# Kernel optimization log

Measured on AMD Instinct MI355X. Metric: run time of the kernel, lower is better.

## Reference

```python
import jax, jax.numpy as jnp
import numpy as np

TEMPERATURE = 1.0


def setup_inputs() -> dict:
    key = jax.random.key(0)
    kq, kk, kv = jax.random.split(key, 3)
    shape = (2, 16, 2048, 64)  # B, H, L, D
    q = jax.random.normal(kq, shape, dtype=jnp.float32)
    k = jax.random.normal(kk, shape, dtype=jnp.float32)
    v = jax.random.normal(kv, shape, dtype=jnp.float32)
    return {"q": q, "k": k, "v": v}


def reference(q, k, v):
    # q, k, v: [B, H, L, D]
    L = q.shape[2]
    # scores: [B, H, L, L]; note: divided by temperature, NOT sqrt(D), per source
    scores = jnp.einsum("bhqd,bhkd->bhqk", q, k) / TEMPERATURE
    # causal mask: position j > i masked with -inf
    causal = jnp.tril(jnp.ones((L, L), dtype=bool))  # True = keep
    scores = jnp.where(causal, scores, -jnp.inf)
    attn = jax.nn.softmax(scores, axis=-1)
    out = jnp.einsum("bhqk,bhkd->bhqd", attn, v)
    return out
```

## Files before the change

kernel.cpp:

```cpp
#include <hip/hip_runtime.h>
#include <math.h>


typedef __attribute__((ext_vector_type(8))) _Float16 f16x8;
typedef __attribute__((ext_vector_type(4))) _Float16 f16x4;
typedef __attribute__((ext_vector_type(4))) float f32x4;

constexpr int Lq = 2048;
constexpr int Dd = 64;
constexpr int KT = 64;
constexpr int THREADS = 256;
constexpr int CHUNK = 64;
constexpr int NCHUNK = Lq / CHUNK;
constexpr int PAIRS = NCHUNK / 2;

#define SWZB(row, bcol) ((((row) * 128) + (bcol)) ^ (((row) & 7) << 4))

__global__ __launch_bounds__(THREADS)
void causal_attn_mfma(const float* __restrict__ Q, const float* __restrict__ K,
                      const float* __restrict__ V, float* __restrict__ O) {
  __shared__ char ks[2][KT * 128];
  __shared__ char vt[2][Dd * 128];
  __shared__ char pl[4][16 * 128];

  const int tid  = threadIdx.x;
  const int lane = tid & 63;
  const int wv   = tid >> 6;
  const int l15  = lane & 15;
  const int g    = lane >> 4;
  const int kg = tid & 15;
  const int dq = tid >> 4;

  const int bh = blockIdx.x / PAIRS;
  const int pr = blockIdx.x % PAIRS;
  const size_t base = (size_t)bh * Lq * Dd;
  const float* Qb = Q + base;
  const float* Kb = K + base;
  const float* Vb = V + base;
  float*       Ob = O + base;
  char* pw = pl[wv];

  #pragma unroll 1
  for (int phase = 0; phase < 2; ++phase) {
    const int chunk = (phase == 0) ? pr : (NCHUNK - 1 - pr);
    const int row0  = chunk * CHUNK;
    const int T     = chunk + 1;
    const int qrow  = row0 + wv * 16;

    f16x8 qf[2];
    #pragma unroll
    for (int kk = 0; kk < 2; ++kk) {
      const float* qp = Qb + (size_t)(qrow + l15) * Dd + kk * 32 + g * 8;
      const f32x4 a = *reinterpret_cast<const f32x4*>(qp);
      const f32x4 b = *reinterpret_cast<const f32x4*>(qp + 4);
      f16x8 q8;
      #pragma unroll
      for (int i = 0; i < 4; ++i) {
        q8[i]     = (_Float16)a[i];
        q8[i + 4] = (_Float16)b[i];
      }
      qf[kk] = q8;
    }

    float m[4], lsum[4];
    f32x4 o[4];
    #pragma unroll
    for (int r = 0; r < 4; ++r) { m[r] = -INFINITY; lsum[r] = 0.f; }
    #pragma unroll
    for (int nd = 0; nd < 4; ++nd) o[nd] = f32x4{0.f, 0.f, 0.f, 0.f};

    {
      f32x4 kreg[4], vreg[4];
      #pragma unroll
      for (int i = 0; i < 4; ++i) {
        const int c = tid + i * 256;
        kreg[i] = *reinterpret_cast<const f32x4*>(
            Kb + (size_t)(c >> 4) * Dd + (c & 15) * 4);
      }
      #pragma unroll
      for (int c = 0; c < 4; ++c) {
        vreg[c] = *reinterpret_cast<const f32x4*>(
            Vb + (size_t)(kg * 4 + c) * Dd + dq * 4);
      }
      __syncthreads();
      #pragma unroll
      for (int i = 0; i < 4; ++i) {
        const int c = tid + i * 256;
        f16x4 h;
        #pragma unroll
        for (int j = 0; j < 4; ++j) h[j] = (_Float16)kreg[i][j];
        *reinterpret_cast<f16x4*>(ks[0] + SWZB(c >> 4, (c & 15) * 8)) = h;
      }
      #pragma unroll
      for (int j = 0; j < 4; ++j) {
        f16x4 h;
        #pragma unroll
        for (int c = 0; c < 4; ++c) h[c] = (_Float16)vreg[c][j];
        *reinterpret_cast<f16x4*>(vt[0] + SWZB(dq * 4 + j, kg * 8)) = h;
      }
    }

    int cur = 0;
    #pragma unroll 1
    for (int t = 0; t < T; ++t) {
      __syncthreads();
      const char* kb = ks[cur];
      const char* vb = vt[cur];

      f32x4 kreg[4], vreg[4];
      const bool pfn = (t + 1 < T);
      if (pfn) {
        const float* Kt = Kb + (size_t)(t + 1) * KT * Dd;
        const float* Vt = Vb + (size_t)(t + 1) * KT * Dd;
        #pragma unroll
        for (int i = 0; i < 4; ++i) {
          const int c = tid + i * 256;
          kreg[i] = *reinterpret_cast<const f32x4*>(
              Kt + (size_t)(c >> 4) * Dd + (c & 15) * 4);
        }
        #pragma unroll
        for (int c = 0; c < 4; ++c) {
          vreg[c] = *reinterpret_cast<const f32x4*>(
              Vt + (size_t)(kg * 4 + c) * Dd + dq * 4);
        }
      }

      f32x4 s[4];
      #pragma unroll
      for (int n = 0; n < 4; ++n) s[n] = f32x4{0.f, 0.f, 0.f, 0.f};
      __builtin_amdgcn_s_setprio(1);
      #pragma unroll
      for (int kk = 0; kk < 2; ++kk) {
        #pragma unroll
        for (int n = 0; n < 4; ++n) {
          const f16x8 kf = *reinterpret_cast<const f16x8*>(
              kb + SWZB(n * 16 + l15, kk * 64 + g * 16));
          s[n] = __builtin_amdgcn_mfma_f32_16x16x32_f16(qf[kk], kf, s[n], 0, 0, 0);
        }
      }
      __builtin_amdgcn_s_setprio(0);

      if (t == T - 1) {
        #pragma unroll
        for (int n = 0; n < 4; ++n) {
          const int key = t * KT + n * 16 + l15;
          #pragma unroll
          for (int r = 0; r < 4; ++r) {
            if (key > qrow + 4 * g + r) s[n][r] = -INFINITY;
          }
        }
      }

      float rmax[4], rsum[4], scale[4];
      #pragma unroll
      for (int r = 0; r < 4; ++r)
        rmax[r] = fmaxf(fmaxf(s[0][r], s[1][r]), fmaxf(s[2][r], s[3][r]));
      #pragma unroll
      for (int mk = 1; mk <= 8; mk <<= 1) {
        #pragma unroll
        for (int r = 0; r < 4; ++r)
          rmax[r] = fmaxf(rmax[r], __shfl_xor(rmax[r], mk));
      }
      #pragma unroll
      for (int r = 0; r < 4; ++r) {
        const float mn = fmaxf(m[r], rmax[r]);
        scale[r] = __expf(m[r] - mn);
        m[r] = mn;
      }
      #pragma unroll
      for (int n = 0; n < 4; ++n) {
        #pragma unroll
        for (int r = 0; r < 4; ++r) s[n][r] = __expf(s[n][r] - m[r]);
      }
      #pragma unroll
      for (int r = 0; r < 4; ++r)
        rsum[r] = (s[0][r] + s[1][r]) + (s[2][r] + s[3][r]);
      #pragma unroll
      for (int mk = 1; mk <= 8; mk <<= 1) {
        #pragma unroll
        for (int r = 0; r < 4; ++r) rsum[r] += __shfl_xor(rsum[r], mk);
      }
      #pragma unroll
      for (int r = 0; r < 4; ++r) lsum[r] = lsum[r] * scale[r] + rsum[r];
      #pragma unroll
      for (int nd = 0; nd < 4; ++nd) {
        #pragma unroll
        for (int r = 0; r < 4; ++r) o[nd][r] *= scale[r];
      }

      #pragma unroll
      for (int n = 0; n < 4; ++n) {
        #pragma unroll
        for (int r = 0; r < 4; ++r) {
          *reinterpret_cast<_Float16*>(
              pw + SWZB(4 * g + r, (n * 16 + l15) * 2)) = (_Float16)s[n][r];
        }
      }
      asm volatile("s_waitcnt lgkmcnt(0)" ::: "memory");
      __builtin_amdgcn_sched_barrier(0);

      __builtin_amdgcn_s_setprio(1);
      #pragma unroll
      for (int kblk = 0; kblk < 2; ++kblk) {
        const f16x8 pf = *reinterpret_cast<const f16x8*>(
            pw + SWZB(l15, kblk * 64 + g * 16));
        #pragma unroll
        for (int nd = 0; nd < 4; ++nd) {
          const f16x8 vf = *reinterpret_cast<const f16x8*>(
              vb + SWZB(nd * 16 + l15, kblk * 64 + g * 16));
          o[nd] = __builtin_amdgcn_mfma_f32_16x16x32_f16(pf, vf, o[nd], 0, 0, 0);
        }
      }
      __builtin_amdgcn_s_setprio(0);

      if (pfn) {
        char* kn = ks[cur ^ 1];
        char* vn = vt[cur ^ 1];
        #pragma unroll
        for (int i = 0; i < 4; ++i) {
          const int c = tid + i * 256;
          f16x4 h;
          #pragma unroll
          for (int j = 0; j < 4; ++j) h[j] = (_Float16)kreg[i][j];
          *reinterpret_cast<f16x4*>(kn + SWZB(c >> 4, (c & 15) * 8)) = h;
        }
        #pragma unroll
        for (int j = 0; j < 4; ++j) {
          f16x4 h;
          #pragma unroll
          for (int c = 0; c < 4; ++c) h[c] = (_Float16)vreg[c][j];
          *reinterpret_cast<f16x4*>(vn + SWZB(dq * 4 + j, kg * 8)) = h;
        }
      }
      cur ^= 1;
    }

    float inv[4];
    #pragma unroll
    for (int r = 0; r < 4; ++r) inv[r] = 1.f / lsum[r];
    #pragma unroll
    for (int nd = 0; nd < 4; ++nd) {
      #pragma unroll
      for (int r = 0; r < 4; ++r) {
        Ob[(size_t)(qrow + 4 * g + r) * Dd + nd * 16 + l15] = o[nd][r] * inv[r];
      }
    }
  }
}

extern "C" void kernel_launch(void* const* d_in, const int* in_sizes, int n_in,
                              void* d_out, int out_size, void* d_ws, size_t ws_size,
                              hipStream_t stream) {
  const float* q = (const float*)d_in[0];
  const float* k = (const float*)d_in[1];
  const float* v = (const float*)d_in[2];
  float* o = (float*)d_out;
  const int bh_count = in_sizes[0] / (Lq * Dd);
  const int grid = bh_count * PAIRS;
  causal_attn_mfma<<<dim3((unsigned)grid), dim3(THREADS), 0, stream>>>(q, k, v, o);
  (void)d_ws; (void)ws_size; (void)n_in; (void)out_size;
}
```

Measured before the change: 84.44 us.

## Pre-convert K/V to fp16 in workspace and stream tiles via global_load_lds

A new prep kernel converts K to fp16 and writes V transposed in fp16 into the workspace. The main kernel then fills its swizzled shared-memory tiles with direct global-to-LDS loads instead of loading fp32 into registers, converting, and storing. It also moves to 512-thread blocks covering 128 query rows, with each wave skipping key tiles past its causal limit. This removes per-tile conversion work and register staging, and halves the bytes each main-kernel pass reads, at the cost of an extra launch, an extra pass over K and V, and fewer, larger blocks. A fallback path keeps the old kernel when the workspace is too small.

```diff
diff --git a/kernel.cpp b/kernel.cpp
--- a/kernel.cpp
+++ b/kernel.cpp
@@ -5,47 +5,115 @@
 typedef __attribute__((ext_vector_type(8))) _Float16 f16x8;
 typedef __attribute__((ext_vector_type(4))) _Float16 f16x4;
 typedef __attribute__((ext_vector_type(4))) float f32x4;
+typedef unsigned short u16;
+typedef __attribute__((ext_vector_type(8))) u16 u16x8;
 
 constexpr int Lq = 2048;
 constexpr int Dd = 64;
 constexpr int KT = 64;
-constexpr int THREADS = 256;
-constexpr int CHUNK = 64;
+constexpr int BH = 32;
+
+#define SWZB(row, bcol) ((((row) * 128) + (bcol)) ^ (((row) & 7) << 4))
+
+#define GLOAD_LDS16(g, l)                                                     \
+  __builtin_amdgcn_global_load_lds(                                           \
+      (const __attribute__((address_space(1))) void*)(g),                     \
+      (__attribute__((address_space(3))) void*)(l), 16, 0, 0)
+
+static __device__ __forceinline__ u16 f2h(float x) {
+  return __builtin_bit_cast(u16, (_Float16)x);
+}
+
+constexpr int PREP_KB = (BH * Lq * Dd) / (256 * 16);
+
+__global__ __launch_bounds__(256)
+void attn_prep(const float* __restrict__ K, const float* __restrict__ V,
+               u16* __restrict__ Kh, u16* __restrict__ VTh) {
+  const int b = blockIdx.x;
+  const int tid = threadIdx.x;
+  if (b < PREP_KB) {
+    const size_t base = ((size_t)b * 256 + tid) * 16;
+    const f32x4* src = reinterpret_cast<const f32x4*>(K + base);
+    u16x8 o0, o1;
+    #pragma unroll
+    for (int i = 0; i < 2; ++i) {
+      const f32x4 a = src[i];
+      #pragma unroll
+      for (int j = 0; j < 4; ++j) o0[i * 4 + j] = f2h(a[j]);
+    }
+    #pragma unroll
+    for (int i = 0; i < 2; ++i) {
+      const f32x4 a = src[2 + i];
+      #pragma unroll
+      for (int j = 0; j < 4; ++j) o1[i * 4 + j] = f2h(a[j]);
+    }
+    *reinterpret_cast<u16x8*>(Kh + base) = o0;
+    *reinterpret_cast<u16x8*>(Kh + base + 8) = o1;
+  } else {
+    __shared__ u16 lt[64][66];
+    const int vb = b - PREP_KB;
+    const int h = vb >> 5, tt = vb & 31;
+    const float* Vt = V + ((size_t)h * Lq + tt * 64) * Dd;
+    const int r = tid & 63, dg = tid >> 6;
+    #pragma unroll
+    for (int i = 0; i < 4; ++i) {
+      const f32x4 a = *reinterpret_cast<const f32x4*>(Vt + (size_t)r * Dd + dg * 16 + i * 4);
+      #pragma unroll
+      for (int j = 0; j < 2; ++j) {
+        const unsigned two =
+            (unsigned)f2h(a[2 * j]) | ((unsigned)f2h(a[2 * j + 1]) << 16);
+        *reinterpret_cast<unsigned*>(&lt[r][dg * 16 + i * 4 + j * 2]) = two;
+      }
+    }
+    __syncthreads();
+    const int d = tid >> 2, kq = tid & 3;
+    u16x8 w0, w1;
+    #pragma unroll
+    for (int j = 0; j < 8; ++j) w0[j] = lt[kq * 16 + j][d];
+    #pragma unroll
+    for (int j = 0; j < 8; ++j) w1[j] = lt[kq * 16 + 8 + j][d];
+    u16* dst = VTh + ((size_t)h * Dd + d) * Lq + tt * 64 + kq * 16;
+    *reinterpret_cast<u16x8*>(dst) = w0;
+    *reinterpret_cast<u16x8*>(dst + 8) = w1;
+  }
+}
+
+constexpr int THREADS = 512;
+constexpr int CHUNK = 128;
 constexpr int NCHUNK = Lq / CHUNK;
 constexpr int PAIRS = NCHUNK / 2;
 
-#define SWZB(row, bcol) ((((row) * 128) + (bcol)) ^ (((row) & 7) << 4))
-
 __global__ __launch_bounds__(THREADS)
-void causal_attn_mfma(const float* __restrict__ Q, const float* __restrict__ K,
-                      const float* __restrict__ V, float* __restrict__ O) {
-  __shared__ char ks[2][KT * 128];
-  __shared__ char vt[2][Dd * 128];
-  __shared__ char pl[4][16 * 128];
+void attn_main(const float* __restrict__ Q, float* __restrict__ O,
+               const u16* __restrict__ Kh, const u16* __restrict__ VTh) {
+  __shared__ char ks[2][8192];
+  __shared__ char vt2[2][8192];
+  __shared__ char pl[8][2048];
 
   const int tid  = threadIdx.x;
   const int lane = tid & 63;
   const int wv   = tid >> 6;
   const int l15  = lane & 15;
   const int g    = lane >> 4;
-  const int kg = tid & 15;
-  const int dq = tid >> 4;
 
   const int bh = blockIdx.x / PAIRS;
   const int pr = blockIdx.x % PAIRS;
-  const size_t base = (size_t)bh * Lq * Dd;
-  const float* Qb = Q + base;
-  const float* Kb = K + base;
-  const float* Vb = V + base;
-  float*       Ob = O + base;
+  const float* Qb = Q + (size_t)bh * Lq * Dd;
+  float*       Ob = O + (size_t)bh * Lq * Dd;
+  const u16*   Kb = Kh + (size_t)bh * Lq * Dd;
+  const u16*   Vb = VTh + (size_t)bh * Dd * Lq;
   char* pw = pl[wv];
+
+  const int lsw = lane ^ ((lane >> 3) & 7);
+  const int r_ = lsw >> 3, s_ = lsw & 7;
 
   #pragma unroll 1
   for (int phase = 0; phase < 2; ++phase) {
     const int chunk = (phase == 0) ? pr : (NCHUNK - 1 - pr);
     const int row0  = chunk * CHUNK;
-    const int T     = chunk + 1;
+    const int T     = 2 * (chunk + 1);
     const int qrow  = row0 + wv * 16;
+    const int tLast = qrow >> 6;
 
     f16x8 qf[2];
     #pragma unroll
@@ -69,44 +137,194 @@
     #pragma unroll
     for (int nd = 0; nd < 4; ++nd) o[nd] = f32x4{0.f, 0.f, 0.f, 0.f};
 
-    {
-      f32x4 kreg[4], vreg[4];
-      #pragma unroll
-      for (int i = 0; i < 4; ++i) {
-        const int c = tid + i * 256;
-        kreg[i] = *reinterpret_cast<const f32x4*>(
-            Kb + (size_t)(c >> 4) * Dd + (c & 15) * 4);
-      }
-      #pragma unroll
-      for (int c = 0; c < 4; ++c) {
-        vreg[c] = *reinterpret_cast<const f32x4*>(
-            Vb + (size_t)(kg * 4 + c) * Dd + dq * 4);
-      }
-      __syncthreads();
-      #pragma unroll
-      for (int i = 0; i < 4; ++i) {
-        const int c = tid + i * 256;
-        f16x4 h;
-        #pragma unroll
-        for (int j = 0; j < 4; ++j) h[j] = (_Float16)kreg[i][j];
-        *reinterpret_cast<f16x4*>(ks[0] + SWZB(c >> 4, (c & 15) * 8)) = h;
-      }
-      #pragma unroll
-      for (int j = 0; j < 4; ++j) {
-        f16x4 h;
-        #pragma unroll
-        for (int c = 0; c < 4; ++c) h[c] = (_Float16)vreg[c][j];
-        *reinterpret_cast<f16x4*>(vt[0] + SWZB(dq * 4 + j, kg * 8)) = h;
-      }
-    }
+    __syncthreads();
+    GLOAD_LDS16(Kb + (size_t)(8 * wv) * Dd + lsw * 8, ks[0] + wv * 1024);
+    GLOAD_LDS16(Vb + (size_t)(8 * wv + r_) * Lq + s_ * 8, vt2[0] + wv * 1024);
 
     int cur = 0;
     #pragma unroll 1
     for (int t = 0; t < T; ++t) {
       __syncthreads();
-      const char* kb = ks[cur];
-      const char* vb = vt[cur];
-
+      if (t + 1 < T) {
+        GLOAD_LDS16(Kb + (size_t)((t + 1) * KT + 8 * wv) * Dd + lsw * 8,
+                    ks[cur ^ 1] + wv * 1024);
+        GLOAD_LDS16(Vb + (size_t)(8 * wv + r_) * Lq + (t + 1) * KT + s_ * 8,
+                    vt2[cur ^ 1] + wv * 1024);
+      }
+      if (t <= tLast) {
+        const char* kb = ks[cur];
+        const char* vb = vt2[cur];
+
+        f32x4 s[4];
+        #pragma unroll
+        for (int n = 0; n < 4; ++n) s[n] = f32x4{0.f, 0.f, 0.f, 0.f};
+        __builtin_amdgcn_s_setprio(1);
+        #pragma unroll
+        for (int kk = 0; kk < 2; ++kk) {
+          #pragma unroll
+          for (int n = 0; n < 4; ++n) {
+            const f16x8 kf = *reinterpret_cast<const f16x8*>(
+                kb + SWZB(n * 16 + l15, kk * 64 + g * 16));
+            s[n] = __builtin_amdgcn_mfma_f32_16x16x32_f16(qf[kk], kf, s[n], 0, 0, 0);
+          }
+        }
+        __builtin_amdgcn_s_setprio(0);
+
+        if (t == tLast) {
+          #pragma unroll
+          for (int n = 0; n < 4; ++n) {
+            const int key = t * KT + n * 16 + l15;
+            #pragma unroll
+            for (int r = 0; r < 4; ++r) {
+              if (key > qrow + 4 * g + r) s[n][r] = -INFINITY;
+            }
+          }
+        }
+
+        float rmax[4], rsum[4], scale[4];
+        #pragma unroll
+        for (int r = 0; r < 4; ++r)
+          rmax[r] = fmaxf(fmaxf(s[0][r], s[1][r]), fmaxf(s[2][r], s[3][r]));
+        #pragma unroll
+        for (int mk = 1; mk <= 8; mk <<= 1) {
+          #pragma unroll
+          for (int r = 0; r < 4; ++r)
+            rmax[r] = fmaxf(rmax[r], __shfl_xor(rmax[r], mk));
+        }
+        #pragma unroll
+        for (int r = 0; r < 4; ++r) {
+          const float mn = fmaxf(m[r], rmax[r]);
+          scale[r] = __expf(m[r] - mn);
+          m[r] = mn;
+        }
+        #pragma unroll
+        for (int n = 0; n < 4; ++n) {
+          #pragma unroll
+          for (int r = 0; r < 4; ++r) s[n][r] = __expf(s[n][r] - m[r]);
+        }
+        #pragma unroll
+        for (int r = 0; r < 4; ++r)
+          rsum[r] = (s[0][r] + s[1][r]) + (s[2][r] + s[3][r]);
+        #pragma unroll
+        for (int mk = 1; mk <= 8; mk <<= 1) {
+          #pragma unroll
+          for (int r = 0; r < 4; ++r) rsum[r] += __shfl_xor(rsum[r], mk);
+        }
+        #pragma unroll
+        for (int r = 0; r < 4; ++r) lsum[r] = lsum[r] * scale[r] + rsum[r];
+        #pragma unroll
+        for (int nd = 0; nd < 4; ++nd) {
+          #pragma unroll
+          for (int r = 0; r < 4; ++r) o[nd][r] *= scale[r];
+        }
+
+        #pragma unroll
+        for (int n = 0; n < 4; ++n) {
+          #pragma unroll
+          for (int r = 0; r < 4; ++r) {
+            *reinterpret_cast<_Float16*>(
+                pw + SWZB(4 * g + r, (n * 16 + l15) * 2)) = (_Float16)s[n][r];
+          }
+        }
+        asm volatile("s_waitcnt lgkmcnt(0)" ::: "memory");
+        __builtin_amdgcn_sched_barrier(0);
+
+        __builtin_amdgcn_s_setprio(1);
+        #pragma unroll
+        for (int kblk = 0; kblk < 2; ++kblk) {
+          const f16x8 pf = *reinterpret_cast<const f16x8*>(
+              pw + SWZB(l15, kblk * 64 + g * 16));
+          #pragma unroll
+          for (int nd = 0; nd < 4; ++nd) {
+            const f16x8 vf = *reinterpret_cast<const f16x8*>(
+                vb + SWZB(nd * 16 + l15, kblk * 64 + g * 16));
+            o[nd] = __builtin_amdgcn_mfma_f32_16x16x32_f16(pf, vf, o[nd], 0, 0, 0);
+          }
+        }
+        __builtin_amdgcn_s_setprio(0);
+      }
+      cur ^= 1;
+    }
+
+    float inv[4];
+    #pragma unroll
+    for (int r = 0; r < 4; ++r) inv[r] = 1.f / lsum[r];
+    #pragma unroll
+    for (int nd = 0; nd < 4; ++nd) {
+      #pragma unroll
+      for (int r = 0; r < 4; ++r) {
+        Ob[(size_t)(qrow + 4 * g + r) * Dd + nd * 16 + l15] = o[nd][r] * inv[r];
+      }
+    }
+  }
+}
+
+__global__ __launch_bounds__(256)
+void causal_attn_fb(const float* __restrict__ Q, const float* __restrict__ K,
+                    const float* __restrict__ V, float* __restrict__ O) {
+  __shared__ char ks[2][KT * 128];
+  __shared__ char vt[2][Dd * 128];
+  __shared__ char pl[4][16 * 128];
+  const int tid = threadIdx.x, lane = tid & 63, wv = tid >> 6;
+  const int l15 = lane & 15, g = lane >> 4;
+  const int kg = tid & 15, dq = tid >> 4;
+  const int bh = blockIdx.x / 16, pr = blockIdx.x % 16;
+  const size_t base = (size_t)bh * Lq * Dd;
+  const float* Qb = Q + base; const float* Kb = K + base;
+  const float* Vb = V + base; float* Ob = O + base;
+  char* pw = pl[wv];
+  #pragma unroll 1
+  for (int phase = 0; phase < 2; ++phase) {
+    const int chunk = (phase == 0) ? pr : (31 - pr);
+    const int row0 = chunk * 64, T = chunk + 1, qrow = row0 + wv * 16;
+    f16x8 qf[2];
+    #pragma unroll
+    for (int kk = 0; kk < 2; ++kk) {
+      const float* qp = Qb + (size_t)(qrow + l15) * Dd + kk * 32 + g * 8;
+      const f32x4 a = *reinterpret_cast<const f32x4*>(qp);
+      const f32x4 b = *reinterpret_cast<const f32x4*>(qp + 4);
+      f16x8 q8;
+      #pragma unroll
+      for (int i = 0; i < 4; ++i) { q8[i] = (_Float16)a[i]; q8[i+4] = (_Float16)b[i]; }
+      qf[kk] = q8;
+    }
+    float m[4], lsum[4]; f32x4 o[4];
+    #pragma unroll
+    for (int r = 0; r < 4; ++r) { m[r] = -INFINITY; lsum[r] = 0.f; }
+    #pragma unroll
+    for (int nd = 0; nd < 4; ++nd) o[nd] = f32x4{0.f, 0.f, 0.f, 0.f};
+    {
+      f32x4 kreg[4], vreg[4];
+      #pragma unroll
+      for (int i = 0; i < 4; ++i) {
+        const int c = tid + i * 256;
+        kreg[i] = *reinterpret_cast<const f32x4*>(Kb + (size_t)(c >> 4) * Dd + (c & 15) * 4);
+      }
+      #pragma unroll
+      for (int c = 0; c < 4; ++c)
+        vreg[c] = *reinterpret_cast<const f32x4*>(Vb + (size_t)(kg * 4 + c) * Dd + dq * 4);
+      __syncthreads();
+      #pragma unroll
+      for (int i = 0; i < 4; ++i) {
+        const int c = tid + i * 256;
+        f16x4 h;
+        #pragma unroll
+        for (int j = 0; j < 4; ++j) h[j] = (_Float16)kreg[i][j];
+        *reinterpret_cast<f16x4*>(ks[0] + SWZB(c >> 4, (c & 15) * 8)) = h;
+      }
+      #pragma unroll
+      for (int j = 0; j < 4; ++j) {
+        f16x4 h;
+        #pragma unroll
+        for (int c = 0; c < 4; ++c) h[c] = (_Float16)vreg[c][j];
+        *reinterpret_cast<f16x4*>(vt[0] + SWZB(dq * 4 + j, kg * 8)) = h;
+      }
+    }
+    int cur = 0;
+    #pragma unroll 1
+    for (int t = 0; t < T; ++t) {
+      __syncthreads();
+      const char* kb = ks[cur]; const char* vb = vt[cur];
       f32x4 kreg[4], vreg[4];
       const bool pfn = (t + 1 < T);
       if (pfn) {
@@ -115,42 +333,32 @@
         #pragma unroll
         for (int i = 0; i < 4; ++i) {
           const int c = tid + i * 256;
-          kreg[i] = *reinterpret_cast<const f32x4*>(
-              Kt + (size_t)(c >> 4) * Dd + (c & 15) * 4);
-        }
-        #pragma unroll
-        for (int c = 0; c < 4; ++c) {
-          vreg[c] = *reinterpret_cast<const f32x4*>(
-              Vt + (size_t)(kg * 4 + c) * Dd + dq * 4);
-        }
-      }
-
+          kreg[i] = *reinterpret_cast<const f32x4*>(Kt + (size_t)(c >> 4) * Dd + (c & 15) * 4);
+        }
+        #pragma unroll
+        for (int c = 0; c < 4; ++c)
+          vreg[c] = *reinterpret_cast<const f32x4*>(Vt + (size_t)(kg * 4 + c) * Dd + dq * 4);
+      }
       f32x4 s[4];
       #pragma unroll
       for (int n = 0; n < 4; ++n) s[n] = f32x4{0.f, 0.f, 0.f, 0.f};
-      __builtin_amdgcn_s_setprio(1);
       #pragma unroll
       for (int kk = 0; kk < 2; ++kk) {
         #pragma unroll
         for (int n = 0; n < 4; ++n) {
-          const f16x8 kf = *reinterpret_cast<const f16x8*>(
-              kb + SWZB(n * 16 + l15, kk * 64 + g * 16));
+          const f16x8 kf = *reinterpret_cast<const f16x8*>(kb + SWZB(n * 16 + l15, kk * 64 + g * 16));
           s[n] = __builtin_amdgcn_mfma_f32_16x16x32_f16(qf[kk], kf, s[n], 0, 0, 0);
         }
       }
-      __builtin_amdgcn_s_setprio(0);
-
       if (t == T - 1) {
         #pragma unroll
         for (int n = 0; n < 4; ++n) {
           const int key = t * KT + n * 16 + l15;
           #pragma unroll
-          for (int r = 0; r < 4; ++r) {
+          for (int r = 0; r < 4; ++r)
             if (key > qrow + 4 * g + r) s[n][r] = -INFINITY;
-          }
-        }
-      }
-
+        }
+      }
       float rmax[4], rsum[4], scale[4];
       #pragma unroll
       for (int r = 0; r < 4; ++r)
@@ -158,14 +366,12 @@
       #pragma unroll
       for (int mk = 1; mk <= 8; mk <<= 1) {
         #pragma unroll
-        for (int r = 0; r < 4; ++r)
-          rmax[r] = fmaxf(rmax[r], __shfl_xor(rmax[r], mk));
+        for (int r = 0; r < 4; ++r) rmax[r] = fmaxf(rmax[r], __shfl_xor(rmax[r], mk));
       }
       #pragma unroll
       for (int r = 0; r < 4; ++r) {
         const float mn = fmaxf(m[r], rmax[r]);
-        scale[r] = __expf(m[r] - mn);
-        m[r] = mn;
+        scale[r] = __expf(m[r] - mn); m[r] = mn;
       }
       #pragma unroll
       for (int n = 0; n < 4; ++n) {
@@ -173,8 +379,7 @@
         for (int r = 0; r < 4; ++r) s[n][r] = __expf(s[n][r] - m[r]);
       }
       #pragma unroll
-      for (int r = 0; r < 4; ++r)
-        rsum[r] = (s[0][r] + s[1][r]) + (s[2][r] + s[3][r]);
+      for (int r = 0; r < 4; ++r) rsum[r] = (s[0][r] + s[1][r]) + (s[2][r] + s[3][r]);
       #pragma unroll
       for (int mk = 1; mk <= 8; mk <<= 1) {
         #pragma unroll
@@ -187,35 +392,25 @@
         #pragma unroll
         for (int r = 0; r < 4; ++r) o[nd][r] *= scale[r];
       }
-
       #pragma unroll
       for (int n = 0; n < 4; ++n) {
         #pragma unroll
-        for (int r = 0; r < 4; ++r) {
-          *reinterpret_cast<_Float16*>(
-              pw + SWZB(4 * g + r, (n * 16 + l15) * 2)) = (_Float16)s[n][r];
-        }
+        for (int r = 0; r < 4; ++r)
+          *reinterpret_cast<_Float16*>(pw + SWZB(4 * g + r, (n * 16 + l15) * 2)) = (_Float16)s[n][r];
       }
       asm volatile("s_waitcnt lgkmcnt(0)" ::: "memory");
       __builtin_amdgcn_sched_barrier(0);
-
-      __builtin_amdgcn_s_setprio(1);
       #pragma unroll
       for (int kblk = 0; kblk < 2; ++kblk) {
-        const f16x8 pf = *reinterpret_cast<const f16x8*>(
-            pw + SWZB(l15, kblk * 64 + g * 16));
+        const f16x8 pf = *reinterpret_cast<const f16x8*>(pw + SWZB(l15, kblk * 64 + g * 16));
         #pragma unroll
         for (int nd = 0; nd < 4; ++nd) {
-          const f16x8 vf = *reinterpret_cast<const f16x8*>(
-              vb + SWZB(nd * 16 + l15, kblk * 64 + g * 16));
+          const f16x8 vf = *reinterpret_cast<const f16x8*>(vb + SWZB(nd * 16 + l15, kblk * 64 + g * 16));
           o[nd] = __builtin_amdgcn_mfma_f32_16x16x32_f16(pf, vf, o[nd], 0, 0, 0);
         }
       }
-      __builtin_amdgcn_s_setprio(0);
-
       if (pfn) {
-        char* kn = ks[cur ^ 1];
-        char* vn = vt[cur ^ 1];
+        char* kn = ks[cur ^ 1]; char* vn = vt[cur ^ 1];
         #pragma unroll
         for (int i = 0; i < 4; ++i) {
           const int c = tid + i * 256;
@@ -234,16 +429,14 @@
       }
       cur ^= 1;
     }
-
     float inv[4];
     #pragma unroll
     for (int r = 0; r < 4; ++r) inv[r] = 1.f / lsum[r];
     #pragma unroll
     for (int nd = 0; nd < 4; ++nd) {
       #pragma unroll
-      for (int r = 0; r < 4; ++r) {
+      for (int r = 0; r < 4; ++r)
         Ob[(size_t)(qrow + 4 * g + r) * Dd + nd * 16 + l15] = o[nd][r] * inv[r];
-      }
     }
   }
 }
@@ -255,8 +448,15 @@
   const float* k = (const float*)d_in[1];
   const float* v = (const float*)d_in[2];
   float* o = (float*)d_out;
-  const int bh_count = in_sizes[0] / (Lq * Dd);
-  const int grid = bh_count * PAIRS;
-  causal_attn_mfma<<<dim3((unsigned)grid), dim3(THREADS), 0, stream>>>(q, k, v, o);
-  (void)d_ws; (void)ws_size; (void)n_in; (void)out_size;
+  const size_t elems = (size_t)BH * Lq * Dd;
+  const size_t need = elems * 2 * 2;
+  if (ws_size >= need) {
+    u16* Kh = (u16*)d_ws;
+    u16* VTh = Kh + elems;
+    attn_prep<<<dim3(2 * PREP_KB), dim3(256), 0, stream>>>(k, v, Kh, VTh);
+    attn_main<<<dim3(BH * PAIRS), dim3(THREADS), 0, stream>>>(q, o, Kh, VTh);
+  } else {
+    causal_attn_fb<<<dim3(BH * 16), dim3(256), 0, stream>>>(q, k, v, o);
+  }
+  (void)in_sizes; (void)n_in; (void)out_size;
 }
```

Result: no change. 84.19 us (-0.3%).
